# Kernel optimization log

Measured on AMD Instinct MI355X. Metric: run time of the kernel, lower is better.

The kernel has to match this reference:

```python
import jax, jax.numpy as jnp
import numpy as np

N_NODES = 10000
N_EDGES = 320000
IN_DIM = 256
OUT_DIM = 256
N_REL = 16


def setup_inputs() -> dict:
    key = jax.random.key(0)
    k_x, k_src, k_dst, k_et, k_wr, k_w0 = jax.random.split(key, 6)
    x = jax.random.normal(k_x, (N_NODES, IN_DIM), dtype=jnp.float32)
    src = jax.random.randint(k_src, (N_EDGES,), 0, N_NODES)
    dst = jax.random.randint(k_dst, (N_EDGES,), 0, N_NODES)
    edge_index = jnp.stack([src, dst], axis=0)  # [2, E]
    edge_type = jax.random.randint(k_et, (N_EDGES,), 0, N_REL)
    # Xavier-uniform-ish init for weights
    lim_r = float(np.sqrt(6.0 / (IN_DIM + OUT_DIM)))
    W_r = jax.random.uniform(k_wr, (N_REL, IN_DIM, OUT_DIM), minval=-lim_r, maxval=lim_r, dtype=jnp.float32)
    W0_w = jax.random.uniform(k_w0, (OUT_DIM, IN_DIM), minval=-lim_r, maxval=lim_r, dtype=jnp.float32)
    W0_b = jnp.zeros((OUT_DIM,), dtype=jnp.float32)
    return {
        "x": x,
        "W_r": W_r,
        "W0_w": W0_w,
        "W0_b": W0_b,
        "edge_index": edge_index,
        "edge_type": edge_type,
        "num_nodes_local": N_NODES,
    }


def reference(x, W_r, W0_w, W0_b, edge_index, edge_type, num_nodes_local):
    N = num_nodes_local
    R = W_r.shape[0]
    src = edge_index[0]
    dst = edge_index[1]
    # Per-(relation, dst-node) in-degree, clamped at 1 (matches deg_r.clamp_min(1))
    deg = jnp.zeros((R, N), dtype=x.dtype).at[edge_type, dst].add(1.0)
    deg = jnp.maximum(deg, 1.0)  # [R, N]
    # Transform all nodes under every relation weight: grouped GEMM [R, N, out]
    h_all = jnp.einsum('nd,rdo->rno', x, W_r)
    # Gather per-edge message and normalize by relation-specific dst degree
    msg = h_all[edge_type, src] / deg[edge_type, dst][:, None]  # [E, out]
    # Scatter-add messages to destination nodes
    agg = jax.ops.segment_sum(msg, dst, num_segments=N)  # [N, out]
    # Self-loop transform W_0(x)
    return agg + x @ W0_w.T + W0_b
```

## Files before the change

kernel.cpp:

```cpp
#include <hip/hip_runtime.h>

typedef __bf16 bf16x8 __attribute__((ext_vector_type(8)));
typedef float f32x4 __attribute__((ext_vector_type(4)));

static __device__ __forceinline__ unsigned short f2bf(float f) {
    union { float f; unsigned int u; } v; v.f = f;
    unsigned int r = v.u + 0x7fffu + ((v.u >> 16) & 1u);
    return (unsigned short)(r >> 16);
}
static __device__ __forceinline__ float blo(unsigned int u) {
    union { unsigned int u; float f; } v; v.u = u << 16; return v.f;
}
static __device__ __forceinline__ float bhi(unsigned int u) {
    union { unsigned int u; float f; } v; v.u = u & 0xffff0000u; return v.f;
}
static __device__ __forceinline__ unsigned int pack2(float a, float b) {
    return (unsigned int)f2bf(a) | ((unsigned int)f2bf(b) << 16);
}

__global__ void zero_kernel(int* __restrict__ p, int n) {
    int i = blockIdx.x * blockDim.x + threadIdx.x;
    int n4 = n >> 2;
    if (i < n4) reinterpret_cast<int4*>(p)[i] = make_int4(0, 0, 0, 0);
    if (i < (n & 3)) p[(n4 << 2) + i] = 0;
}

__global__ void prep_kernel(const int* __restrict__ dst, const int* __restrict__ et,
                            int* __restrict__ deg, int* __restrict__ eoff,
                            const float* __restrict__ x, unsigned short* __restrict__ s,
                            int E, int N, int R, int nh) {
    const int bid = blockIdx.x, tid = threadIdx.x;
    const int K = (R + 1) * 256;
    if (bid < nh) {
        int i = bid * 256 + tid;
        if (i < E) eoff[i] = atomicAdd(&deg[et[i] * N + dst[i]], 1);
    } else {
        int id = (bid - nh) * 256 + tid;
        int n = id >> 6, c4 = id & 63;
        if (n < N) {
            float4 v = *reinterpret_cast<const float4*>(&x[((size_t)n << 8) + (c4 << 2)]);
            ushort4 h;
            h.x = f2bf(v.x); h.y = f2bf(v.y); h.z = f2bf(v.z); h.w = f2bf(v.w);
            *reinterpret_cast<ushort4*>(&s[(size_t)n * K + (K - 256) + (c4 << 2)]) = h;
        }
    }
}

__global__ __launch_bounds__(256) void wtT_kernel(
    const float* __restrict__ Wr, const float* __restrict__ W0w,
    unsigned short* __restrict__ Wt2, int R, int K)
{
    __shared__ float t[64][65];
    const int sl = blockIdx.x, d0 = blockIdx.y * 64, o0 = blockIdx.z * 64;
    const int tid = threadIdx.x;
    if (sl < R) {
        #pragma unroll
        for (int j = 0; j < 16; ++j) {
            int idx = j * 256 + tid;
            int dr = idx >> 6, oc = idx & 63;
            t[dr][oc] = Wr[((size_t)sl * 256 + d0 + dr) * 256 + o0 + oc];
        }
        __syncthreads();
        #pragma unroll
        for (int j = 0; j < 4; ++j) {
            int idx = j * 256 + tid;
            int orow = idx >> 4, dc4 = (idx & 15) << 2;
            ushort4 h;
            h.x = f2bf(t[dc4 + 0][orow]); h.y = f2bf(t[dc4 + 1][orow]);
            h.z = f2bf(t[dc4 + 2][orow]); h.w = f2bf(t[dc4 + 3][orow]);
            *reinterpret_cast<ushort4*>(&Wt2[(size_t)(o0 + orow) * K + sl * 256 + d0 + dc4]) = h;
        }
    } else {
        #pragma unroll
        for (int j = 0; j < 4; ++j) {
            int idx = j * 256 + tid;
            int orow = idx >> 4, dc4 = (idx & 15) << 2;
            float4 v = *reinterpret_cast<const float4*>(&W0w[(size_t)(o0 + orow) * 256 + d0 + dc4]);
            ushort4 h;
            h.x = f2bf(v.x); h.y = f2bf(v.y); h.z = f2bf(v.z); h.w = f2bf(v.w);
            *reinterpret_cast<ushort4*>(&Wt2[(size_t)(o0 + orow) * K + sl * 256 + d0 + dc4]) = h;
        }
    }
}

__global__ void scan1_kernel(const int* __restrict__ deg, int* __restrict__ local,
                             int* __restrict__ bsum, int B) {
    __shared__ int tmp[256];
    int t = threadIdx.x, g = blockIdx.x * 256 + t;
    int v = (g < B) ? deg[g] : 0;
    tmp[t] = v; __syncthreads();
    for (int o = 1; o < 256; o <<= 1) {
        int u = (t >= o) ? tmp[t - o] : 0;
        __syncthreads();
        tmp[t] += u;
        __syncthreads();
    }
    if (g < B) local[g] = tmp[t] - v;
    if (t == 255) bsum[blockIdx.x] = tmp[t];
}

__global__ void scan2_kernel(const int* __restrict__ bsum, int* __restrict__ base, int nc) {
    __shared__ int tmp[1024];
    int t = threadIdx.x;
    int v = (t < nc) ? bsum[t] : 0;
    tmp[t] = v; __syncthreads();
    for (int o = 1; o < 1024; o <<= 1) {
        int u = (t >= o) ? tmp[t - o] : 0;
        __syncthreads();
        tmp[t] += u;
        __syncthreads();
    }
    if (t < nc) base[t] = tmp[t] - v;
}

__global__ void scatter_ids_kernel(const int* __restrict__ src, const int* __restrict__ dst,
                                   const int* __restrict__ et, const int* __restrict__ local,
                                   const int* __restrict__ base, const int* __restrict__ eoff,
                                   int* __restrict__ srcs, int E, int N) {
    int i = blockIdx.x * blockDim.x + threadIdx.x;
    if (i < E) {
        int b = et[i] * N + dst[i];
        srcs[local[b] + base[b >> 8] + eoff[i]] = src[i];
    }
}

__global__ __launch_bounds__(256) void reduce_kernel(
    const int* __restrict__ srcs, const int* __restrict__ deg,
    const int* __restrict__ local, const int* __restrict__ base,
    unsigned short* __restrict__ s, int N, int R)
{
    const int K = (R + 1) * 256;
    const int r = blockIdx.y;
    const int dn = blockIdx.x * 8 + (threadIdx.x >> 5);
    if (dn >= N) return;
    const int lane = threadIdx.x & 31;
    const int bin = r * N + dn;
    const int cnt = deg[bin];
    const int st  = local[bin] + base[bin >> 8];

    float a0 = 0.f, a1 = 0.f, a2 = 0.f, a3 = 0.f;
    float a4 = 0.f, a5 = 0.f, a6 = 0.f, a7 = 0.f;
    for (int c0 = 0; c0 < cnt; c0 += 32) {
        int sv = 0;
        if (c0 + lane < cnt) sv = srcs[st + c0 + lane];
        int m = cnt - c0; if (m > 32) m = 32;
        for (int i = 0; i < m; ++i) {
            int sn = __shfl(sv, i, 32);
            const uint4 v = *reinterpret_cast<const uint4*>(
                &s[(size_t)sn * K + (K - 256) + (lane << 3)]);
            a0 += blo(v.x); a1 += bhi(v.x);
            a2 += blo(v.y); a3 += bhi(v.y);
            a4 += blo(v.z); a5 += bhi(v.z);
            a6 += blo(v.w); a7 += bhi(v.w);
        }
    }
    if (cnt > 0) {
        float sc = 1.0f / (float)cnt;
        a0 *= sc; a1 *= sc; a2 *= sc; a3 *= sc;
        a4 *= sc; a5 *= sc; a6 *= sc; a7 *= sc;
    }
    uint4 o;
    o.x = pack2(a0, a1); o.y = pack2(a2, a3);
    o.z = pack2(a4, a5); o.w = pack2(a6, a7);
    *reinterpret_cast<uint4*>(&s[(size_t)dn * K + (r << 8) + (lane << 3)]) = o;
}

__global__ __launch_bounds__(256) void gemm_kernel(
    const unsigned short* __restrict__ S, const unsigned short* __restrict__ Wt2,
    const float* __restrict__ bias, float* __restrict__ dest,
    int M, int K, int ksteps, int addbias)
{
    __shared__ __align__(16) unsigned short ldsA[2][8192];
    __shared__ __align__(16) unsigned short ldsB[8192];
    const int tid = threadIdx.x;
    const int lane = tid & 63, w = tid >> 6;
    const int wm = w & 1, wn = w >> 1;
    const int m0 = blockIdx.x * 128, n0 = blockIdx.y * 128;
    const int kstart = blockIdx.z * ksteps * 64;
    const size_t rowb = (size_t)K * 2;

    f32x4 acc[4][4] = {};

    const int flat_base = w * 4 * 64 + lane;

#define STAGE_A(buf, kstep)                                                               \
    {                                                                                     \
        const int kb = (kstart + (kstep) * 64) * 2;                                       \
        _Pragma("unroll")                                                                 \
        for (int i = 0; i < 4; ++i) {                                                     \
            int flat = flat_base + i * 64;                                                \
            int row = flat >> 3, seg = flat & 7;                                          \
            int gr = m0 + row; gr = gr < M ? gr : M - 1;                                  \
            const char* gp = (const char*)S + (size_t)gr * rowb + kb                      \
                             + ((seg * 16) ^ ((row & 7) << 4));                           \
            unsigned short* lp = &ldsA[buf][(w * 4 + i) * 512];                           \
            __builtin_amdgcn_global_load_lds(                                             \
                (const __attribute__((address_space(1))) void*)gp,                        \
                (__attribute__((address_space(3))) void*)lp, 16, 0, 0);                   \
        }                                                                                 \
    }

#define STAGE_B(kstep)                                                                    \
    {                                                                                     \
        const int kb = (kstart + (kstep) * 64) * 2;                                       \
        _Pragma("unroll")                                                                 \
        for (int i = 0; i < 4; ++i) {                                                     \
            int flat = flat_base + i * 64;                                                \
            int row = flat >> 3, seg = flat & 7;                                          \
            const char* gp = (const char*)Wt2 + (size_t)(n0 + row) * rowb + kb            \
                             + ((seg * 16) ^ ((row & 7) << 4));                           \
            unsigned short* lp = &ldsB[(w * 4 + i) * 512];                                \
            __builtin_amdgcn_global_load_lds(                                             \
                (const __attribute__((address_space(1))) void*)gp,                        \
                (__attribute__((address_space(3))) void*)lp, 16, 0, 0);                   \
        }                                                                                 \
    }

#define COMPUTE(buf)                                                                      \
    {                                                                                     \
        _Pragma("unroll")                                                                 \
        for (int kk = 0; kk < 2; ++kk) {                                                  \
            bf16x8 af[4], bfr[4];                                                         \
            _Pragma("unroll")                                                             \
            for (int m = 0; m < 4; ++m) {                                                 \
                int row = wm * 64 + m * 16 + (lane & 15);                                 \
                int colb = (kk * 64 + ((lane >> 4) << 4)) ^ ((row & 7) << 4);             \
                af[m] = *reinterpret_cast<const bf16x8*>(                                 \
                    (const char*)&ldsA[buf][0] + row * 128 + colb);                       \
            }                                                                             \
            _Pragma("unroll")                                                             \
            for (int n = 0; n < 4; ++n) {                                                 \
                int row = wn * 64 + n * 16 + (lane & 15);                                 \
                int colb = (kk * 64 + ((lane >> 4) << 4)) ^ ((row & 7) << 4);             \
                bfr[n] = *reinterpret_cast<const bf16x8*>(                                \
                    (const char*)&ldsB[0] + row * 128 + colb);                            \
            }                                                                             \
            __builtin_amdgcn_s_setprio(1);                                                \
            _Pragma("unroll")                                                             \
            for (int m = 0; m < 4; ++m)                                                   \
                _Pragma("unroll")                                                         \
                for (int n = 0; n < 4; ++n)                                               \
                    acc[m][n] = __builtin_amdgcn_mfma_f32_16x16x32_bf16(                  \
                        af[m], bfr[n], acc[m][n], 0, 0, 0);                               \
            __builtin_amdgcn_s_setprio(0);                                                \
        }                                                                                 \
    }

    STAGE_A(0, 0)
    STAGE_B(0)
    STAGE_A(1, 1)
    asm volatile("s_waitcnt vmcnt(4)" ::: "memory");
    __builtin_amdgcn_s_barrier();

    for (int t = 0; t < ksteps; ++t) {
        COMPUTE(t & 1)
        asm volatile("s_waitcnt lgkmcnt(0)" ::: "memory");
        __builtin_amdgcn_sched_barrier(0);
        __builtin_amdgcn_s_barrier();
        if (t + 1 < ksteps) {
            STAGE_B(t + 1)
            if (t + 2 < ksteps) {
                STAGE_A(t & 1, t + 2)
                asm volatile("s_waitcnt vmcnt(4)" ::: "memory");
            } else {
                asm volatile("s_waitcnt vmcnt(0)" ::: "memory");
            }
            __builtin_amdgcn_s_barrier();
        }
    }
#undef STAGE_A
#undef STAGE_B
#undef COMPUTE

    float* dst = dest + (size_t)blockIdx.z * M * 256;
    if (addbias) dst = dest;
    const int rbase = m0 + wm * 64 + ((lane >> 4) << 2);
    const int cbase = n0 + wn * 64 + (lane & 15);
    #pragma unroll
    for (int n = 0; n < 4; ++n) {
        int c = cbase + n * 16;
        float bv = addbias ? bias[c] : 0.0f;
        #pragma unroll
        for (int m = 0; m < 4; ++m) {
            #pragma unroll
            for (int j = 0; j < 4; ++j) {
                int r = rbase + m * 16 + j;
                if (r < M) dst[(size_t)r * 256 + c] = acc[m][n][j] + bv;
            }
        }
    }
}

__global__ void combine_kernel(const float* __restrict__ pbuf, const float* __restrict__ bias,
                               float* __restrict__ out, int M, int KZ) {
    int id = blockIdx.x * blockDim.x + threadIdx.x;
    if (id >= M * 64) return;
    int n = id >> 6, c4 = id & 63;
    float4 a = *reinterpret_cast<const float4*>(&pbuf[((size_t)n << 8) + (c4 << 2)]);
    for (int kz = 1; kz < KZ; ++kz) {
        float4 b = *reinterpret_cast<const float4*>(&pbuf[(size_t)kz * M * 256 + ((size_t)n << 8) + (c4 << 2)]);
        a.x += b.x; a.y += b.y; a.z += b.z; a.w += b.w;
    }
    const float4 bv = *reinterpret_cast<const float4*>(&bias[c4 << 2]);
    a.x += bv.x; a.y += bv.y; a.z += bv.z; a.w += bv.w;
    *reinterpret_cast<float4*>(&out[((size_t)n << 8) + (c4 << 2)]) = a;
}

extern "C" void kernel_launch(void* const* d_in, const int* in_sizes, int n_in,
                              void* d_out, int out_size, void* d_ws, size_t ws_size,
                              hipStream_t stream) {
    const float* x   = (const float*)d_in[0];
    const float* Wr  = (const float*)d_in[1];
    const float* W0w = (const float*)d_in[2];
    const float* W0b = (const float*)d_in[3];
    const int*   eidx= (const int*)d_in[4];
    const int*   et  = (const int*)d_in[5];
    const int N = in_sizes[0] / 256;
    const int R = in_sizes[1] / 65536;
    const int E = in_sizes[5];
    const int* src = eidx;
    const int* dst = eidx + E;
    float* out = (float*)d_out;

    const int B = R * N;
    const int NC = (B + 255) / 256;
    const int K = (R + 1) * 256;

    const size_t sz_pslice = (size_t)N * 256 * 4;
    const size_t sz_sort = (((size_t)B * 4 + 255) & ~255UL) * 2
                         + (((size_t)E * 4 + 255) & ~255UL) * 2
                         + 2 * 4096;
    const size_t sz_wt2 = (size_t)256 * K * 2;
    const size_t sz_s   = (size_t)N * K * 2;
    int KZ = 1;
    for (int kz = 4; kz >= 1; kz >>= 1) {
        size_t r0 = (kz > 1) ? (size_t)kz * sz_pslice : 0;
        if (sz_sort > r0) r0 = sz_sort;
        size_t need = ((r0 + 255) & ~255UL) + ((sz_wt2 + 255) & ~255UL) + sz_s + 1024;
        if (need <= ws_size || kz == 1) { KZ = kz; break; }
    }

    char* ws = (char*)d_ws;
    size_t off = 0;
    auto alloc = [&](size_t bytes) { void* p = ws + off; off = (off + bytes + 255) & ~(size_t)255; return p; };
    float* pbuf = (float*)ws;
    int* deg    = (int*)alloc((size_t)B * 4);
    int* local  = (int*)alloc((size_t)B * 4);
    int* bsum   = (int*)alloc(4096);
    int* base   = (int*)alloc(4096);
    int* eoff   = (int*)alloc((size_t)E * 4);
    int* srcs   = (int*)alloc((size_t)E * 4);
    size_t region0 = (KZ > 1) ? (size_t)KZ * sz_pslice : 0;
    if (off > region0) region0 = off;
    off = (region0 + 255) & ~(size_t)255;
    unsigned short* Wt2 = (unsigned short*)alloc(sz_wt2);
    unsigned short* s   = (unsigned short*)alloc(sz_s);

    zero_kernel<<<(B / 4 + 255) / 256, 256, 0, stream>>>(deg, B);
    {
        const int nh = (E + 255) / 256;
        const int nx = (N * 64 + 255) / 256;
        prep_kernel<<<nh + nx, 256, 0, stream>>>(dst, et, deg, eoff, x, s, E, N, R, nh);
    }
    {
        dim3 gw(R + 1, 4, 4);
        wtT_kernel<<<gw, 256, 0, stream>>>(Wr, W0w, Wt2, R, K);
    }
    scan1_kernel<<<NC, 256, 0, stream>>>(deg, local, bsum, B);
    scan2_kernel<<<1, 1024, 0, stream>>>(bsum, base, NC);
    scatter_ids_kernel<<<(E + 255) / 256, 256, 0, stream>>>(src, dst, et, local, base, eoff, srcs, E, N);
    {
        dim3 g((N + 7) / 8, R);
        reduce_kernel<<<g, 256, 0, stream>>>(srcs, deg, local, base, s, N, R);
    }
    {
        const int ktot = K / 64;
        const int ksteps = ktot / KZ;
        dim3 grid((N + 127) / 128, 2, KZ);
        if (KZ == 1) {
            gemm_kernel<<<grid, 256, 0, stream>>>(s, Wt2, W0b, out, N, K, ksteps, 1);
        } else {
            gemm_kernel<<<grid, 256, 0, stream>>>(s, Wt2, W0b, pbuf, N, K, ksteps, 0);
            combine_kernel<<<(N * 64 + 255) / 256, 256, 0, stream>>>(pbuf, W0b, out, N, KZ);
        }
    }
}
```

Measured before the change: 124.2 us.

## Fuse weight transpose into prep kernel and remap GEMM blocks XCD-aware

Merges the weight transpose/bf16 conversion kernel into the prep kernel as extra blocks, removing one launch and letting it overlap with the degree and x conversion work. The GEMM grid is reordered so N-tiles vary fastest, and block IDs are remapped round-robin across 8 groups (XCDs) so blocks sharing A rows land on the same chiplet for L2 reuse. The prep kernel now reserves 16.6KB of shared memory even for blocks that don't use it, which may lower occupancy for the atomic path.

```diff
diff --git a/kernel.cpp b/kernel.cpp
--- a/kernel.cpp
+++ b/kernel.cpp
@@ -25,16 +25,21 @@
     if (i < (n & 3)) p[(n4 << 2) + i] = 0;
 }
 
-__global__ void prep_kernel(const int* __restrict__ dst, const int* __restrict__ et,
-                            int* __restrict__ deg, int* __restrict__ eoff,
-                            const float* __restrict__ x, unsigned short* __restrict__ s,
-                            int E, int N, int R, int nh) {
+__global__ __launch_bounds__(256) void prep_kernel(
+    const int* __restrict__ dst, const int* __restrict__ et,
+    int* __restrict__ deg, int* __restrict__ eoff,
+    const float* __restrict__ x, unsigned short* __restrict__ s,
+    const float* __restrict__ Wr, const float* __restrict__ W0w,
+    unsigned short* __restrict__ Wt2,
+    int E, int N, int R, int nh, int nx)
+{
+    __shared__ float t[64][65];
     const int bid = blockIdx.x, tid = threadIdx.x;
     const int K = (R + 1) * 256;
     if (bid < nh) {
         int i = bid * 256 + tid;
         if (i < E) eoff[i] = atomicAdd(&deg[et[i] * N + dst[i]], 1);
-    } else {
+    } else if (bid < nh + nx) {
         int id = (bid - nh) * 256 + tid;
         int n = id >> 6, c4 = id & 63;
         if (n < N) {
@@ -43,42 +48,36 @@
             h.x = f2bf(v.x); h.y = f2bf(v.y); h.z = f2bf(v.z); h.w = f2bf(v.w);
             *reinterpret_cast<ushort4*>(&s[(size_t)n * K + (K - 256) + (c4 << 2)]) = h;
         }
-    }
-}
-
-__global__ __launch_bounds__(256) void wtT_kernel(
-    const float* __restrict__ Wr, const float* __restrict__ W0w,
-    unsigned short* __restrict__ Wt2, int R, int K)
-{
-    __shared__ float t[64][65];
-    const int sl = blockIdx.x, d0 = blockIdx.y * 64, o0 = blockIdx.z * 64;
-    const int tid = threadIdx.x;
-    if (sl < R) {
-        #pragma unroll
-        for (int j = 0; j < 16; ++j) {
-            int idx = j * 256 + tid;
-            int dr = idx >> 6, oc = idx & 63;
-            t[dr][oc] = Wr[((size_t)sl * 256 + d0 + dr) * 256 + o0 + oc];
-        }
-        __syncthreads();
-        #pragma unroll
-        for (int j = 0; j < 4; ++j) {
-            int idx = j * 256 + tid;
-            int orow = idx >> 4, dc4 = (idx & 15) << 2;
-            ushort4 h;
-            h.x = f2bf(t[dc4 + 0][orow]); h.y = f2bf(t[dc4 + 1][orow]);
-            h.z = f2bf(t[dc4 + 2][orow]); h.w = f2bf(t[dc4 + 3][orow]);
-            *reinterpret_cast<ushort4*>(&Wt2[(size_t)(o0 + orow) * K + sl * 256 + d0 + dc4]) = h;
-        }
     } else {
-        #pragma unroll
-        for (int j = 0; j < 4; ++j) {
-            int idx = j * 256 + tid;
-            int orow = idx >> 4, dc4 = (idx & 15) << 2;
-            float4 v = *reinterpret_cast<const float4*>(&W0w[(size_t)(o0 + orow) * 256 + d0 + dc4]);
-            ushort4 h;
-            h.x = f2bf(v.x); h.y = f2bf(v.y); h.z = f2bf(v.z); h.w = f2bf(v.w);
-            *reinterpret_cast<ushort4*>(&Wt2[(size_t)(o0 + orow) * K + sl * 256 + d0 + dc4]) = h;
+        int tb = bid - nh - nx;
+        int sl = tb >> 4, d0 = ((tb >> 2) & 3) * 64, o0 = (tb & 3) * 64;
+        if (sl < R) {
+            #pragma unroll
+            for (int j = 0; j < 16; ++j) {
+                int idx = j * 256 + tid;
+                int dr = idx >> 6, oc = idx & 63;
+                t[dr][oc] = Wr[((size_t)sl * 256 + d0 + dr) * 256 + o0 + oc];
+            }
+            __syncthreads();
+            #pragma unroll
+            for (int j = 0; j < 4; ++j) {
+                int idx = j * 256 + tid;
+                int orow = idx >> 4, dc4 = (idx & 15) << 2;
+                ushort4 h;
+                h.x = f2bf(t[dc4 + 0][orow]); h.y = f2bf(t[dc4 + 1][orow]);
+                h.z = f2bf(t[dc4 + 2][orow]); h.w = f2bf(t[dc4 + 3][orow]);
+                *reinterpret_cast<ushort4*>(&Wt2[(size_t)(o0 + orow) * K + sl * 256 + d0 + dc4]) = h;
+            }
+        } else {
+            #pragma unroll
+            for (int j = 0; j < 4; ++j) {
+                int idx = j * 256 + tid;
+                int orow = idx >> 4, dc4 = (idx & 15) << 2;
+                float4 v = *reinterpret_cast<const float4*>(&W0w[(size_t)(o0 + orow) * 256 + d0 + dc4]);
+                ushort4 h;
+                h.x = f2bf(v.x); h.y = f2bf(v.y); h.z = f2bf(v.z); h.w = f2bf(v.w);
+                *reinterpret_cast<ushort4*>(&Wt2[(size_t)(o0 + orow) * K + sl * 256 + d0 + dc4]) = h;
+            }
         }
     }
 }
@@ -175,8 +174,15 @@
     const int tid = threadIdx.x;
     const int lane = tid & 63, w = tid >> 6;
     const int wm = w & 1, wn = w >> 1;
-    const int m0 = blockIdx.x * 128, n0 = blockIdx.y * 128;
-    const int kstart = blockIdx.z * ksteps * 64;
+
+    const int nM = gridDim.y;
+    const int nwg = 2 * nM * gridDim.z;
+    int L = blockIdx.x + 2 * (blockIdx.y + nM * blockIdx.z);
+    if ((nwg & 7) == 0) { int q = nwg >> 3; L = (L & 7) * q + (L >> 3); }
+    const int z = L / (2 * nM);
+    const int rem = L - z * (2 * nM);
+    const int m0 = (rem >> 1) * 128, n0 = (rem & 1) * 128;
+    const int kstart = z * ksteps * 64;
     const size_t rowb = (size_t)K * 2;
 
     f32x4 acc[4][4] = {};
@@ -272,7 +278,7 @@
 #undef STAGE_B
 #undef COMPUTE
 
-    float* dst = dest + (size_t)blockIdx.z * M * 256;
+    float* dst = dest + (size_t)z * M * 256;
     if (addbias) dst = dest;
     const int rbase = m0 + wm * 64 + ((lane >> 4) << 2);
     const int cbase = n0 + wn * 64 + (lane & 15);
@@ -360,11 +366,9 @@
     {
         const int nh = (E + 255) / 256;
         const int nx = (N * 64 + 255) / 256;
-        prep_kernel<<<nh + nx, 256, 0, stream>>>(dst, et, deg, eoff, x, s, E, N, R, nh);
-    }
-    {
-        dim3 gw(R + 1, 4, 4);
-        wtT_kernel<<<gw, 256, 0, stream>>>(Wr, W0w, Wt2, R, K);
+        const int nwT = (R + 1) * 16;
+        prep_kernel<<<nh + nx + nwT, 256, 0, stream>>>(dst, et, deg, eoff, x, s,
+                                                       Wr, W0w, Wt2, E, N, R, nh, nx);
     }
     scan1_kernel<<<NC, 256, 0, stream>>>(deg, local, bsum, B);
     scan2_kernel<<<1, 1024, 0, stream>>>(bsum, base, NC);
@@ -376,7 +380,8 @@
     {
         const int ktot = K / 64;
         const int ksteps = ktot / KZ;
-        dim3 grid((N + 127) / 128, 2, KZ);
+        const int nM = (N + 127) / 128;
+        dim3 grid(2, nM, KZ);
         if (KZ == 1) {
             gemm_kernel<<<grid, 256, 0, stream>>>(s, Wt2, W0b, out, N, K, ksteps, 1);
         } else {
```

After: 119.3 us. -4.0%, faster.
